# Kernel optimization log

Measured on AMD Instinct MI355X. Metric: run time of the kernel, lower is better.

The kernel has to match this reference:

```python
import jax, jax.numpy as jnp
import numpy as np

EPS = 1e-5

def _conv1x1(w, x):
    # w: [out,in], x: [b,in,h,w] -> [b,out,h,w]
    return jnp.einsum('oi,bihw->bohw', w, x)

def _aggregate(resp, persp, t_w, p_w, g_w, z_w, gamma, beta):
    t = _conv1x1(t_w, persp)                      # b,c,h,w
    b, c, h, w = t.shape
    tq = t.reshape(b, c, h * w).transpose(0, 2, 1)            # b,N,c
    p = _conv1x1(p_w, resp).reshape(b, c, -1)                 # b,c,M
    g = _conv1x1(g_w, resp).reshape(b, c, -1).transpose(0, 2, 1)  # b,M,c
    att = jax.nn.softmax(jnp.einsum('bnc,bcm->bnm', tq, p), axis=2)  # b,N,M
    out = jnp.einsum('bnm,bmc->bnc', att, g)                  # b,N,c
    # faithful to torch: .contiguous().view(b,c,h,w) with NO permute
    out = out.reshape(b, c, h, w)
    z = _conv1x1(z_w, out)                                    # b,Cp,h,w
    mean = z.mean(axis=(0, 2, 3), keepdims=True)
    var = z.var(axis=(0, 2, 3), keepdims=True)                # biased (train-mode BN)
    zn = (z - mean) / jnp.sqrt(var + EPS)
    return zn * gamma[None, :, None, None] + beta[None, :, None, None]

def setup_inputs() -> dict:
    key = jax.random.key(0)
    ks = jax.random.split(key, 32)
    Cp, Cr, planes = 256, [64, 256, 512, 1024, 2048], 64
    hw = [48, 48, 24, 12, 6]
    d = {}
    d['perspective'] = jax.random.normal(ks[0], (4, Cp, 48, 48), jnp.float32)
    for i in range(5):
        d[f'response{i}'] = jax.random.normal(ks[1 + i], (4, Cr[i], hw[i], hw[i]), jnp.float32)
    d['t_w'] = jax.random.normal(ks[6], (planes, Cp), jnp.float32) * 0.05
    d['z_w'] = jax.random.normal(ks[7], (Cp, planes), jnp.float32) * 0.05
    for i in range(5):
        d[f'p{i}_w'] = jax.random.normal(ks[8 + 2 * i], (planes, Cr[i]), jnp.float32) * 0.05
        d[f'g{i}_w'] = jax.random.normal(ks[9 + 2 * i], (planes, Cr[i]), jnp.float32) * 0.05
        d[f'bn{i}_g'] = jnp.ones((Cp,), jnp.float32)
        d[f'bn{i}_b'] = jnp.zeros((Cp,), jnp.float32)
    return d

def reference(perspective, response0, response1, response2, response3, response4,
              t_w, z_w,
              p0_w, g0_w, bn0_g, bn0_b,
              p1_w, g1_w, bn1_g, bn1_b,
              p2_w, g2_w, bn2_g, bn2_b,
              p3_w, g3_w, bn3_g, bn3_b,
              p4_w, g4_w, bn4_g, bn4_b):
    resps = [response0, response1, response2, response3, response4]
    ps = [p0_w, p1_w, p2_w, p3_w, p4_w]
    gs = [g0_w, g1_w, g2_w, g3_w, g4_w]
    gms = [bn0_g, bn1_g, bn2_g, bn3_g, bn4_g]
    bts = [bn0_b, bn1_b, bn2_b, bn3_b, bn4_b]
    out = None
    for i in range(5):
        o = _aggregate(resps[i], perspective, t_w, ps[i], gs[i], z_w, gms[i], bts[i])
        out = o if out is None else out + o
    return out
```

## Files before the change

kernel.cpp:

```cpp
#include <hip/hip_runtime.h>
#include <hip/hip_bf16.h>
#include <string.h>

#define BB 4
#define CPc 256
#define NN 2304

typedef __attribute__((ext_vector_type(8))) short bf16x8;
typedef __attribute__((ext_vector_type(4))) float f32x4;

__device__ __forceinline__ short f2b(float x) {
    __hip_bfloat16 h = __float2bfloat16(x);
    return *reinterpret_cast<short*>(&h);
}
__device__ __forceinline__ float b2f16(short v) {
    union { float f; unsigned u; } x;
    x.u = ((unsigned)(unsigned short)v) << 16;
    return x.f;
}

__global__ __launch_bounds__(256) void k_wcvt(
    const float* __restrict__ t_w, const float* __restrict__ z_w,
    const float* p0, const float* p1, const float* p2, const float* p3, const float* p4,
    const float* g0, const float* g1, const float* g2, const float* g3, const float* g4,
    short* __restrict__ TWb, short* __restrict__ ZWb,
    short* __restrict__ WPb, short* __restrict__ WGb) {
    int idx = blockIdx.x * 256 + threadIdx.x;
    if (idx < 16384) { TWb[idx] = f2b(t_w[idx]); return; }
    if (idx < 32768) { ZWb[idx - 16384] = f2b(z_w[idx - 16384]); return; }
    int k = idx - 32768;
    bool isP = k < 249856;
    if (!isP) k -= 249856;
    int i, off;
    if (k < 4096)        { i = 0; off = 0; }
    else if (k < 20480)  { i = 1; off = 4096; }
    else if (k < 53248)  { i = 2; off = 20480; }
    else if (k < 118784) { i = 3; off = 53248; }
    else                 { i = 4; off = 118784; }
    const float* s;
    if (isP) s = (i == 0) ? p0 : (i == 1) ? p1 : (i == 2) ? p2 : (i == 3) ? p3 : p4;
    else     s = (i == 0) ? g0 : (i == 1) ? g1 : (i == 2) ? g2 : (i == 3) ? g3 : g4;
    (isP ? WPb : WGb)[k] = f2b(s[k - off]);
}

__global__ __launch_bounds__(256) void k_conv(
    const float* __restrict__ persp,
    const float* r0, const float* r1, const float* r2, const float* r3, const float* r4,
    const short* __restrict__ TWb, const short* __restrict__ WPb, const short* __restrict__ WGb,
    short* __restrict__ TQb, short* __restrict__ PTb, short* __restrict__ GTb,
    float* __restrict__ PPART, float* __restrict__ GPART) {
    const int CUM[7]  = {0, 144, 288, 432, 504, 552, 584};
    const int CRs[6]  = {256, 64, 256, 512, 1024, 2048};
    const int Mus[6]  = {2304, 2304, 2304, 576, 144, 36};
    const int Mps[6]  = {2304, 2304, 2304, 576, 192, 64};
    const int KSs[6]  = {1, 1, 1, 2, 4, 8};
    const int WOFF[6] = {0, 0, 4096, 20480, 53248, 118784};
    const int POFF[6] = {0, 0, 589824, 1179648, 1327104, 1376256};
    const int PBASE[6] = {0, 0, 0, 0, 294912, 491520};

    __shared__ __align__(16) short s_a[64][72];

    int blk = blockIdx.x, t = threadIdx.x;
    int w = t >> 6, lane = t & 63, lo = lane & 15, quad = lane >> 4;
    int seg = 0;
#pragma unroll
    for (int s_ = 1; s_ <= 5; ++s_) if (blk >= CUM[s_]) seg = s_;
    int Cr = CRs[seg], M = Mus[seg], Mp = Mps[seg], KS = KSs[seg];
    const float* in = (seg == 0) ? persp : (seg == 1) ? r0 : (seg == 2) ? r1 :
                      (seg == 3) ? r2 : (seg == 4) ? r3 : r4;
    const short* wp = (seg == 0) ? TWb : WPb + WOFF[seg];
    const short* wg = WGb + WOFF[seg];
    bool has_g = (seg != 0);
    int local = blk - CUM[seg];
    int mt = Mp >> 6;
    int b = local / (mt * KS);
    int rem = local % (mt * KS);
    int m0 = (rem / KS) * 64;
    int ksi = rem % KS;
    int kLen = Cr / KS, k0 = ksi * kLen;

    int ml = t & 63;
    int ssw = (ml >> 3) & 7;
    bool mvalid = (m0 + ml) < M;
    const float* inB = in + ((size_t)b * Cr) * M + m0 + ml;

    int mrow = w * 16 + lo;
    int rsw = (mrow >> 3) & 7;

    f32x4 accP[4], accG[4];
#pragma unroll
    for (int ct = 0; ct < 4; ++ct) {
        accP[ct] = f32x4{0.f, 0.f, 0.f, 0.f};
        accG[ct] = f32x4{0.f, 0.f, 0.f, 0.f};
    }

    for (int kc = k0; kc < k0 + kLen; kc += 64) {
        __syncthreads();
#pragma unroll
        for (int r = 0; r < 8; ++r) {
            int kp = (t >> 6) + r * 4;
            int q = kp >> 2, l = kp & 3;
            float v0 = 0.f, v1 = 0.f;
            if (mvalid) {
                v0 = inB[(size_t)(kc + 2 * kp) * M];
                v1 = inB[(size_t)(kc + 2 * kp + 1) * M];
            }
            short2 pk; pk.x = f2b(v0); pk.y = f2b(v1);
            *(short2*)&s_a[ml][(q ^ ssw) * 8 + l * 2] = pk;
        }
        __syncthreads();
        const bf16x8 fr0 = *(const bf16x8*)&s_a[mrow][8 * (quad ^ rsw)];
        const bf16x8 fr1 = *(const bf16x8*)&s_a[mrow][8 * ((4 + quad) ^ rsw)];
#pragma unroll
        for (int ct = 0; ct < 4; ++ct) {
            const bf16x8 fp0 = *(const bf16x8*)&wp[(size_t)(ct * 16 + lo) * Cr + kc + quad * 8];
            const bf16x8 fp1 = *(const bf16x8*)&wp[(size_t)(ct * 16 + lo) * Cr + kc + 32 + quad * 8];
            accP[ct] = __builtin_amdgcn_mfma_f32_16x16x32_bf16(fr0, fp0, accP[ct], 0, 0, 0);
            accP[ct] = __builtin_amdgcn_mfma_f32_16x16x32_bf16(fr1, fp1, accP[ct], 0, 0, 0);
            if (has_g) {
                const bf16x8 fg0 = *(const bf16x8*)&wg[(size_t)(ct * 16 + lo) * Cr + kc + quad * 8];
                const bf16x8 fg1 = *(const bf16x8*)&wg[(size_t)(ct * 16 + lo) * Cr + kc + 32 + quad * 8];
                accG[ct] = __builtin_amdgcn_mfma_f32_16x16x32_bf16(fg0, fr0, accG[ct], 0, 0, 0);
                accG[ct] = __builtin_amdgcn_mfma_f32_16x16x32_bf16(fg1, fr1, accG[ct], 0, 0, 0);
            }
        }
    }
    if (KS == 1) {
        short* outP = (seg == 0) ? TQb : PTb + POFF[seg];
        short* outG = GTb + POFF[seg];
        int mP = m0 + w * 16 + quad * 4;
#pragma unroll
        for (int ct = 0; ct < 4; ++ct) {
            int c = ct * 16 + lo;
#pragma unroll
            for (int rg = 0; rg < 4; ++rg)
                outP[((size_t)b * Mp + mP + rg) * 64 + c] = f2b(accP[ct][rg]);
        }
        if (has_g) {
            int mG = m0 + w * 16 + lo;
#pragma unroll
            for (int ct = 0; ct < 4; ++ct) {
                int cG = ct * 16 + quad * 4;
#pragma unroll
                for (int rg = 0; rg < 4; ++rg)
                    outG[((size_t)b * 64 + cG + rg) * Mp + mG] = f2b(accG[ct][rg]);
            }
        }
    } else {
        int NP = 4 * Mp * 64;
        float* pp = PPART + PBASE[seg] + (size_t)ksi * NP;
        float* gp = GPART + PBASE[seg] + (size_t)ksi * NP;
        int mP = m0 + w * 16 + quad * 4;
#pragma unroll
        for (int ct = 0; ct < 4; ++ct) {
            int c = ct * 16 + lo;
#pragma unroll
            for (int rg = 0; rg < 4; ++rg)
                pp[((size_t)b * Mp + mP + rg) * 64 + c] = accP[ct][rg];
        }
        int mG = m0 + w * 16 + lo;
#pragma unroll
        for (int ct = 0; ct < 4; ++ct) {
            int cG = ct * 16 + quad * 4;
#pragma unroll
            for (int rg = 0; rg < 4; ++rg)
                gp[((size_t)b * 64 + cG + rg) * Mp + mG] = accG[ct][rg];
        }
    }
}

__global__ __launch_bounds__(256) void k_cvt(const float* __restrict__ PPART,
                                             const float* __restrict__ GPART,
                                             short* __restrict__ PTb, short* __restrict__ GTb) {
    const int EC[4]    = {0, 147456, 196608, 212992};
    const int KSv[3]   = {2, 4, 8};
    const int PBASEv[3] = {0, 294912, 491520};
    const int POFFv[3] = {1179648, 1327104, 1376256};
    int e = blockIdx.x * 256 + threadIdx.x;
    int sg = (e < EC[1]) ? 0 : (e < EC[2]) ? 1 : 2;
    int rem = e - EC[sg];
    int KS = KSv[sg];
    int NP = (sg == 0) ? 147456 : (sg == 1) ? 49152 : 16384;
    {
        const float* src = PPART + PBASEv[sg] + rem;
        float p = 0.f;
        for (int s = 0; s < KS; ++s) p += src[(size_t)s * NP];
        PTb[POFFv[sg] + rem] = f2b(p);
    }
    {
        const float* src = GPART + PBASEv[sg] + rem;
        float g = 0.f;
        for (int s = 0; s < KS; ++s) g += src[(size_t)s * NP];
        GTb[POFFv[sg] + rem] = f2b(g);
    }
}

__global__ __launch_bounds__(256) void k_attn(const short* __restrict__ tq,
                                              const short* __restrict__ PTb,
                                              const short* __restrict__ GTb,
                                              short* __restrict__ OUTb) {
    const int AM[5]    = {2304, 2304, 576, 144, 36};
    const int AMp[5]   = {2304, 2304, 576, 192, 64};
    const int APOFF[5] = {0, 589824, 1179648, 1327104, 1376256};

    __shared__ __align__(16) short s_P[2][32][72];
    __shared__ float s_l[4][32];

    int t = threadIdx.x;
    int seg = blockIdx.x / 288;
    int r = blockIdx.x % 288;
    int b = r / 72;
    int n0 = (r % 72) * 32;
    int M = AM[seg], Mp = AMp[seg];
    const short* pT = PTb + APOFF[seg];
    const short* gT = GTb + APOFF[seg];
    short* outm = OUTb + (size_t)seg * 589824;

    int w = t >> 6, lane = t & 63, lo = lane & 15, quad = lane >> 4;
    bool domask = (M != Mp);

    const short* tqB = tq + ((size_t)b * NN + n0 + lo) * 64 + quad * 8;
    bf16x8 bq[2][2];
#pragma unroll
    for (int i = 0; i < 2; ++i)
#pragma unroll
        for (int h = 0; h < 2; ++h)
            bq[i][h] = *(const bf16x8*)(tqB + i * 16 * 64 + h * 32);

    const short* pA = pT + ((size_t)b * Mp + w * 16 + lo) * 64 + quad * 8;
    const short* gB = gT + ((size_t)b * 64 + w * 16 + lo) * Mp + quad * 8;

    bf16x8 pa0 = *(const bf16x8*)(pA);
    bf16x8 pa1 = *(const bf16x8*)(pA + 32);
    bf16x8 gb0 = *(const bf16x8*)(gB);
    bf16x8 gb1 = *(const bf16x8*)(gB + 32);

    f32x4 accO[2];
    accO[0] = f32x4{0.f, 0.f, 0.f, 0.f};
    accO[1] = f32x4{0.f, 0.f, 0.f, 0.f};
    float lsum[2] = {0.f, 0.f};

    int nch = Mp >> 6;
    for (int ch = 0; ch < nch; ++ch) {
        int m0 = ch << 6;
        bf16x8 pa0n, pa1n, gb0n, gb1n;
        bool more = (ch + 1 < nch);
        if (more) {
            int mn = m0 + 64;
            pa0n = *(const bf16x8*)(pA + (size_t)mn * 64);
            pa1n = *(const bf16x8*)(pA + (size_t)mn * 64 + 32);
            gb0n = *(const bf16x8*)(gB + mn);
            gb1n = *(const bf16x8*)(gB + mn + 32);
        }
        f32x4 S[2];
        S[0] = f32x4{0.f, 0.f, 0.f, 0.f};
        S[0] = __builtin_amdgcn_mfma_f32_16x16x32_bf16(pa0, bq[0][0], S[0], 0, 0, 0);
        S[0] = __builtin_amdgcn_mfma_f32_16x16x32_bf16(pa1, bq[0][1], S[0], 0, 0, 0);
        S[1] = f32x4{0.f, 0.f, 0.f, 0.f};
        S[1] = __builtin_amdgcn_mfma_f32_16x16x32_bf16(pa0, bq[1][0], S[1], 0, 0, 0);
        S[1] = __builtin_amdgcn_mfma_f32_16x16x32_bf16(pa1, bq[1][1], S[1], 0, 0, 0);
        if (domask) {
#pragma unroll
            for (int rg = 0; rg < 4; ++rg) {
                bool oob = (m0 + w * 16 + quad * 4 + rg) >= M;
                if (oob) { S[0][rg] = -1e30f; S[1][rg] = -1e30f; }
            }
        }
        short (*sp)[72] = s_P[ch & 1];
#pragma unroll
        for (int i = 0; i < 2; ++i) {
            short4 pw;
#pragma unroll
            for (int rg = 0; rg < 4; ++rg) {
                float e = __expf(S[i][rg] - 40.f);
                lsum[i] += e;
                ((short*)&pw)[rg] = f2b(e);
            }
            *(short4*)&sp[i * 16 + lo][w * 16 + quad * 4] = pw;
        }
        __syncthreads();
#pragma unroll
        for (int i = 0; i < 2; ++i) {
            const bf16x8 a0 = *(const bf16x8*)&sp[i * 16 + lo][quad * 8];
            const bf16x8 a1 = *(const bf16x8*)&sp[i * 16 + lo][32 + quad * 8];
            accO[i] = __builtin_amdgcn_mfma_f32_16x16x32_bf16(a0, gb0, accO[i], 0, 0, 0);
            accO[i] = __builtin_amdgcn_mfma_f32_16x16x32_bf16(a1, gb1, accO[i], 0, 0, 0);
        }
        if (more) { pa0 = pa0n; pa1 = pa1n; gb0 = gb0n; gb1 = gb1n; }
    }
#pragma unroll
    for (int i = 0; i < 2; ++i) {
        lsum[i] += __shfl_xor(lsum[i], 16, 64);
        lsum[i] += __shfl_xor(lsum[i], 32, 64);
    }
    if (quad == 0) { s_l[w][lo] = lsum[0]; s_l[w][16 + lo] = lsum[1]; }
    __syncthreads();
#pragma unroll
    for (int i = 0; i < 2; ++i)
#pragma unroll
        for (int rg = 0; rg < 4; ++rg) {
            int n = i * 16 + quad * 4 + rg;
            float lt = s_l[0][n] + s_l[1][n] + s_l[2][n] + s_l[3][n];
            outm[((size_t)b * NN + n0 + n) * 64 + w * 16 + lo] = f2b(accO[i][rg] / lt);
        }
}

__global__ __launch_bounds__(256) void k_z(const short* __restrict__ OUTb,
                                           const short* __restrict__ ZWb,
                                           short* __restrict__ Zb,
                                           float* __restrict__ PART) {
    __shared__ __align__(16) short s_ut[64][72];
    int t = threadIdx.x;
    int seg = blockIdx.x / 144;
    int r = blockIdx.x % 144;
    int b = r / 36;
    int sp0 = (r % 36) * 64;
    const short* F = OUTb + (size_t)seg * 589824 + (size_t)b * 147456;
    short* z = Zb + (size_t)seg * 2359296 + (size_t)b * 589824;
    float* part = PART + (size_t)(seg * 144 + r) * 512;

    int w = t >> 6, lane = t & 63, lo = lane & 15, quad = lane >> 4;

    bf16x8 af[4][2];
#pragma unroll
    for (int qt = 0; qt < 4; ++qt)
#pragma unroll
        for (int h = 0; h < 2; ++h)
            af[qt][h] = *(const bf16x8*)&ZWb[(size_t)(w * 64 + qt * 16 + lo) * 64 + h * 32 + quad * 8];

#pragma unroll
    for (int rr = 0; rr < 4; ++rr) {
        int idx = t + rr * 256;
        int spl = idx & 63;
        int cp0 = (idx >> 6) << 2;
        short4 pk;
        pk.x = F[(size_t)(cp0 + 0) * 2304 + sp0 + spl];
        pk.y = F[(size_t)(cp0 + 1) * 2304 + sp0 + spl];
        pk.z = F[(size_t)(cp0 + 2) * 2304 + sp0 + spl];
        pk.w = F[(size_t)(cp0 + 3) * 2304 + sp0 + spl];
        *(short4*)&s_ut[spl][cp0] = pk;
    }
    __syncthreads();

    bf16x8 bfr[4][2];
#pragma unroll
    for (int st = 0; st < 4; ++st)
#pragma unroll
        for (int h = 0; h < 2; ++h)
            bfr[st][h] = *(const bf16x8*)&s_ut[st * 16 + lo][h * 32 + quad * 8];

    f32x4 acc[4][4];
#pragma unroll
    for (int qt = 0; qt < 4; ++qt)
#pragma unroll
        for (int st = 0; st < 4; ++st) {
            acc[qt][st] = f32x4{0.f, 0.f, 0.f, 0.f};
            acc[qt][st] = __builtin_amdgcn_mfma_f32_16x16x32_bf16(af[qt][0], bfr[st][0], acc[qt][st], 0, 0, 0);
            acc[qt][st] = __builtin_amdgcn_mfma_f32_16x16x32_bf16(af[qt][1], bfr[st][1], acc[qt][st], 0, 0, 0);
        }

#pragma unroll
    for (int qt = 0; qt < 4; ++qt) {
        float s1[4] = {0.f, 0.f, 0.f, 0.f};
        float s2[4] = {0.f, 0.f, 0.f, 0.f};
        int qb = w * 64 + qt * 16 + quad * 4;
#pragma unroll
        for (int st = 0; st < 4; ++st) {
            int sp = sp0 + st * 16 + lo;
#pragma unroll
            for (int rg = 0; rg < 4; ++rg) {
                float v = acc[qt][st][rg];
                z[(size_t)(qb + rg) * 2304 + sp] = f2b(v);
                s1[rg] += v;
                s2[rg] += v * v;
            }
        }
#pragma unroll
        for (int rg = 0; rg < 4; ++rg) {
            for (int o = 8; o >= 1; o >>= 1) {
                s1[rg] += __shfl_xor(s1[rg], o, 16);
                s2[rg] += __shfl_xor(s2[rg], o, 16);
            }
            if (lo == 0) {
                float2 v2; v2.x = s1[rg]; v2.y = s2[rg];
                *(float2*)&part[(size_t)(qb + rg) * 2] = v2;
            }
        }
    }
}

__global__ __launch_bounds__(256) void k_stats(const float* __restrict__ PART,
                                               float* __restrict__ STATS) {
    int seg = blockIdx.x;
    int q = threadIdx.x;
    const float* p = PART + (size_t)seg * 144 * 512 + q * 2;
    float s1 = 0.f, s2 = 0.f;
#pragma unroll 16
    for (int blk = 0; blk < 144; ++blk) {
        float2 v = *(const float2*)&p[(size_t)blk * 512];
        s1 += v.x; s2 += v.y;
    }
    STATS[seg * 512 + q * 2] = s1;
    STATS[seg * 512 + q * 2 + 1] = s2;
}

__global__ __launch_bounds__(256) void k_final(
    const short* __restrict__ Zb, const float* __restrict__ STATS,
    const float* g0, const float* g1, const float* g2, const float* g3, const float* g4,
    const float* b0, const float* b1, const float* b2, const float* b3, const float* b4,
    float* __restrict__ outp) {
    int idx4 = (blockIdx.x * 256 + threadIdx.x) * 4;
    int q = (idx4 / NN) & 255;
    const float inv = 1.f / (float)(BB * NN);
    float4 o = {0.f, 0.f, 0.f, 0.f};
#pragma unroll
    for (int i = 0; i < 5; ++i) {
        float mean = STATS[i * 512 + q * 2] * inv;
        float var = STATS[i * 512 + q * 2 + 1] * inv - mean * mean;
        float rr = rsqrtf(var + 1e-5f);
        const float* gm = (i == 0) ? g0 : (i == 1) ? g1 : (i == 2) ? g2 : (i == 3) ? g3 : g4;
        const float* bt = (i == 0) ? b0 : (i == 1) ? b1 : (i == 2) ? b2 : (i == 3) ? b3 : b4;
        float sc = rr * gm[q];
        float ofs = bt[q] - mean * sc;
        short4 zv = *(const short4*)&Zb[(size_t)i * 2359296 + idx4];
        o.x += b2f16(zv.x) * sc + ofs;
        o.y += b2f16(zv.y) * sc + ofs;
        o.z += b2f16(zv.z) * sc + ofs;
        o.w += b2f16(zv.w) * sc + ofs;
    }
    *(float4*)&outp[idx4] = o;
}

extern "C" void kernel_launch(void* const* d_in, const int* in_sizes, int n_in,
                              void* d_out, int out_size, void* d_ws, size_t ws_size,
                              hipStream_t stream) {
    const float* persp = (const float*)d_in[0];
    const float* resp[5];
    for (int i = 0; i < 5; ++i) resp[i] = (const float*)d_in[1 + i];
    const float* t_w = (const float*)d_in[6];
    const float* z_w = (const float*)d_in[7];
    const float *p_w[5], *g_w[5], *bng[5], *bnb[5];
    for (int i = 0; i < 5; ++i) {
        p_w[i] = (const float*)d_in[8 + 4 * i];
        g_w[i] = (const float*)d_in[9 + 4 * i];
        bng[i] = (const float*)d_in[10 + 4 * i];
        bnb[i] = (const float*)d_in[11 + 4 * i];
    }
    short* TQb = (short*)d_ws;
    short* TWb = TQb + 589824;
    short* ZWb = TWb + 16384;
    short* WPb = ZWb + 16384;
    short* WGb = WPb + 249856;
    short* PTb = WGb + 249856;
    short* GTb = PTb + 1392640;
    short* Zb  = GTb + 1392640;
    short* OUTb  = (short*)((float*)d_ws + 7852032);
    float* STATS = (float*)d_ws + 7852032 + 2949120;
    float* PPART = STATS + 2560;
    float* GPART = PPART + 622592;

    k_wcvt<<<2080, 256, 0, stream>>>(t_w, z_w,
        p_w[0], p_w[1], p_w[2], p_w[3], p_w[4],
        g_w[0], g_w[1], g_w[2], g_w[3], g_w[4],
        TWb, ZWb, WPb, WGb);
    k_conv<<<584, 256, 0, stream>>>(persp,
        resp[0], resp[1], resp[2], resp[3], resp[4],
        TWb, WPb, WGb, TQb, PTb, GTb, PPART, GPART);
    k_cvt<<<832, 256, 0, stream>>>(PPART, GPART, PTb, GTb);
    k_attn<<<1440, 256, 0, stream>>>(TQb, PTb, GTb, OUTb);
    k_z<<<720, 256, 0, stream>>>(OUTb, ZWb, Zb, PPART);
    k_stats<<<5, 256, 0, stream>>>(PPART, STATS);
    k_final<<<2304, 256, 0, stream>>>(Zb, STATS,
        bng[0], bng[1], bng[2], bng[3], bng[4],
        bnb[0], bnb[1], bnb[2], bnb[3], bnb[4],
        (float*)d_out);
}
```

Before: 239.4 us.

## Split attention key dimension across four blocks for large segments with combine kernel

```diff
diff --git a/kernel.cpp b/kernel.cpp
--- a/kernel.cpp
+++ b/kernel.cpp
@@ -198,7 +198,9 @@
 __global__ __launch_bounds__(256) void k_attn(const short* __restrict__ tq,
                                               const short* __restrict__ PTb,
                                               const short* __restrict__ GTb,
-                                              short* __restrict__ OUTb) {
+                                              short* __restrict__ OUTb,
+                                              float* __restrict__ PNUM,
+                                              float* __restrict__ PL) {
     const int AM[5]    = {2304, 2304, 576, 144, 36};
     const int AMp[5]   = {2304, 2304, 576, 192, 64};
     const int APOFF[5] = {0, 589824, 1179648, 1327104, 1376256};
@@ -207,17 +209,24 @@
     __shared__ float s_l[4][32];
 
     int t = threadIdx.x;
-    int seg = blockIdx.x / 288;
-    int r = blockIdx.x % 288;
+    int bid = blockIdx.x;
+    int seg, r, p;
+    if (bid < 2304) { seg = bid / 1152; int wi = bid % 1152; p = wi / 288; r = wi % 288; }
+    else            { int q = bid - 2304; seg = 2 + q / 288; r = q % 288; p = 0; }
     int b = r / 72;
     int n0 = (r % 72) * 32;
     int M = AM[seg], Mp = AMp[seg];
     const short* pT = PTb + APOFF[seg];
     const short* gT = GTb + APOFF[seg];
-    short* outm = OUTb + (size_t)seg * 589824;
 
     int w = t >> 6, lane = t & 63, lo = lane & 15, quad = lane >> 4;
     bool domask = (M != Mp);
+    bool split = (seg < 2);
+
+    int nch_tot = Mp >> 6;
+    int c0, c1;
+    if (split) { c0 = p * 9; c1 = c0 + 9; }
+    else       { c0 = 0; c1 = nch_tot; }
 
     const short* tqB = tq + ((size_t)b * NN + n0 + lo) * 64 + quad * 8;
     bf16x8 bq[2][2];
@@ -230,25 +239,25 @@
     const short* pA = pT + ((size_t)b * Mp + w * 16 + lo) * 64 + quad * 8;
     const short* gB = gT + ((size_t)b * 64 + w * 16 + lo) * Mp + quad * 8;
 
-    bf16x8 pa0 = *(const bf16x8*)(pA);
-    bf16x8 pa1 = *(const bf16x8*)(pA + 32);
-    bf16x8 gb0 = *(const bf16x8*)(gB);
-    bf16x8 gb1 = *(const bf16x8*)(gB + 32);
+    size_t m00 = (size_t)c0 << 6;
+    bf16x8 pa0 = *(const bf16x8*)(pA + m00 * 64);
+    bf16x8 pa1 = *(const bf16x8*)(pA + m00 * 64 + 32);
+    bf16x8 gb0 = *(const bf16x8*)(gB + m00);
+    bf16x8 gb1 = *(const bf16x8*)(gB + m00 + 32);
 
     f32x4 accO[2];
     accO[0] = f32x4{0.f, 0.f, 0.f, 0.f};
     accO[1] = f32x4{0.f, 0.f, 0.f, 0.f};
     float lsum[2] = {0.f, 0.f};
 
-    int nch = Mp >> 6;
-    for (int ch = 0; ch < nch; ++ch) {
+    for (int ch = c0; ch < c1; ++ch) {
         int m0 = ch << 6;
         bf16x8 pa0n, pa1n, gb0n, gb1n;
-        bool more = (ch + 1 < nch);
+        bool more = (ch + 1 < c1);
         if (more) {
-            int mn = m0 + 64;
-            pa0n = *(const bf16x8*)(pA + (size_t)mn * 64);
-            pa1n = *(const bf16x8*)(pA + (size_t)mn * 64 + 32);
+            size_t mn = (size_t)(m0 + 64);
+            pa0n = *(const bf16x8*)(pA + mn * 64);
+            pa1n = *(const bf16x8*)(pA + mn * 64 + 32);
             gb0n = *(const bf16x8*)(gB + mn);
             gb1n = *(const bf16x8*)(gB + mn + 32);
         }
@@ -295,14 +304,56 @@
     }
     if (quad == 0) { s_l[w][lo] = lsum[0]; s_l[w][16 + lo] = lsum[1]; }
     __syncthreads();
-#pragma unroll
-    for (int i = 0; i < 2; ++i)
-#pragma unroll
-        for (int rg = 0; rg < 4; ++rg) {
-            int n = i * 16 + quad * 4 + rg;
-            float lt = s_l[0][n] + s_l[1][n] + s_l[2][n] + s_l[3][n];
-            outm[((size_t)b * NN + n0 + n) * 64 + w * 16 + lo] = f2b(accO[i][rg] / lt);
-        }
+    if (split) {
+        float* np = PNUM + ((size_t)((seg * 4 + p) * 288 + r)) * 2048;
+        float* lp = PL + ((size_t)((seg * 4 + p) * 288 + r)) * 32;
+#pragma unroll
+        for (int i = 0; i < 2; ++i)
+#pragma unroll
+            for (int rg = 0; rg < 4; ++rg) {
+                int n = i * 16 + quad * 4 + rg;
+                np[n * 64 + w * 16 + lo] = accO[i][rg];
+                if (w == 0 && lo == 0) {
+                    float lt = s_l[0][n] + s_l[1][n] + s_l[2][n] + s_l[3][n];
+                    lp[n] = lt;
+                }
+            }
+    } else {
+        short* outm = OUTb + (size_t)seg * 589824;
+#pragma unroll
+        for (int i = 0; i < 2; ++i)
+#pragma unroll
+            for (int rg = 0; rg < 4; ++rg) {
+                int n = i * 16 + quad * 4 + rg;
+                float lt = s_l[0][n] + s_l[1][n] + s_l[2][n] + s_l[3][n];
+                outm[((size_t)b * NN + n0 + n) * 64 + w * 16 + lo] = f2b(accO[i][rg] / lt);
+            }
+    }
+}
+
+__global__ __launch_bounds__(256) void k_comb(const float* __restrict__ PNUM,
+                                              const float* __restrict__ PL,
+                                              short* __restrict__ OUTb) {
+    int e4 = (blockIdx.x * 256 + threadIdx.x) * 4;
+    int s = e4 / 589824;
+    int rem = e4 % 589824;
+    int r = rem / 2048;
+    int off = rem % 2048;
+    int n = off >> 6;
+    float ax = 0.f, ay = 0.f, az = 0.f, aw = 0.f, l = 0.f;
+#pragma unroll
+    for (int pp = 0; pp < 4; ++pp) {
+        size_t blkb = (size_t)((s * 4 + pp) * 288 + r);
+        const float4 v = *(const float4*)&PNUM[blkb * 2048 + off];
+        ax += v.x; ay += v.y; az += v.z; aw += v.w;
+        l += PL[blkb * 32 + n];
+    }
+    short4 o;
+    o.x = f2b(ax / l);
+    o.y = f2b(ay / l);
+    o.z = f2b(az / l);
+    o.w = f2b(aw / l);
+    *(short4*)&OUTb[e4] = o;
 }
 
 __global__ __launch_bounds__(256) void k_z(const short* __restrict__ OUTb,
@@ -458,6 +509,8 @@
     float* STATS = (float*)d_ws + 7852032 + 2949120;
     float* PPART = STATS + 2560;
     float* GPART = PPART + 622592;
+    float* PNUM = (float*)Zb;
+    float* PL   = PNUM + 4718592;
 
     k_wcvt<<<2080, 256, 0, stream>>>(t_w, z_w,
         p_w[0], p_w[1], p_w[2], p_w[3], p_w[4],
@@ -467,7 +520,8 @@
         resp[0], resp[1], resp[2], resp[3], resp[4],
         TWb, WPb, WGb, TQb, PTb, GTb, PPART, GPART);
     k_cvt<<<832, 256, 0, stream>>>(PPART, GPART, PTb, GTb);
-    k_attn<<<1440, 256, 0, stream>>>(TQb, PTb, GTb, OUTb);
+    k_attn<<<3168, 256, 0, stream>>>(TQb, PTb, GTb, OUTb, PNUM, PL);
+    k_comb<<<1152, 256, 0, stream>>>(PNUM, PL, OUTb);
     k_z<<<720, 256, 0, stream>>>(OUTb, ZWb, Zb, PPART);
     k_stats<<<5, 256, 0, stream>>>(PPART, STATS);
     k_final<<<2304, 256, 0, stream>>>(Zb, STATS,
```

After: 244.2 us. 2.0% more time.
